# Kernel tuning notes

Hardware: AMD Instinct MI355X
Metric: run time of the kernel (lower is better)

The kernel has to match this reference:

```python
import jax, jax.numpy as jnp
import numpy as np

NB_NEIGHBORS = 8
RADIUS = 0.5
SPLIT = 32
FEATURE_SIZE = 128
OUTPUT_SIZE = 64
MIDDLE = (FEATURE_SIZE + OUTPUT_SIZE) // 2  # 96
N = 100000


def setup_inputs() -> dict:
    key = jax.random.key(0)
    ks = jax.random.split(key, 8)
    points = jax.random.normal(ks[0], (N, 3), dtype=jnp.float32)
    features = jax.random.normal(ks[1], (N, SPLIT + FEATURE_SIZE), dtype=jnp.float32)
    batch = jnp.sort(jax.random.randint(ks[2], (N,), 0, 16)).astype(jnp.int64)
    # neighborhood decoder modeled as Linear(split -> nb_neighbors*3)
    dec_W = jax.random.normal(ks[3], (SPLIT, NB_NEIGHBORS * 3), dtype=jnp.float32) / np.sqrt(SPLIT)
    dec_b = jnp.zeros((NB_NEIGHBORS * 3,), dtype=jnp.float32)
    fc1_W = jax.random.normal(ks[4], (FEATURE_SIZE + 3, MIDDLE), dtype=jnp.float32) / np.sqrt(FEATURE_SIZE + 3)
    fc1_b = jnp.zeros((MIDDLE,), dtype=jnp.float32)
    fc2_W = jax.random.normal(ks[5], (MIDDLE, OUTPUT_SIZE), dtype=jnp.float32) / np.sqrt(MIDDLE)
    fc2_b = jnp.zeros((OUTPUT_SIZE,), dtype=jnp.float32)
    return {"points": points, "features": features, "batch": batch,
            "dec_W": dec_W, "dec_b": dec_b,
            "fc1_W": fc1_W, "fc1_b": fc1_b,
            "fc2_W": fc2_W, "fc2_b": fc2_b}


def reference(points, features, batch, dec_W, dec_b, fc1_W, fc1_b, fc2_W, fc2_b):
    # split incoming features
    point_features = features[:, :SPLIT]            # [N, split] -> neighborhood decoder
    feature_features = features[:, SPLIT:]          # [N, feature_size]
    # neighborhood decoder: nb_neighbors relative 3-D points per input point
    relative_points = (point_features @ dec_W + dec_b).reshape(-1, 3)   # [N*nb, 3]
    output_batch = jnp.repeat(batch, NB_NEIGHBORS, axis=0)              # [N*nb]
    # gather features to each generated neighbor, concat with relative coords
    features_repeated = jnp.repeat(feature_features, NB_NEIGHBORS, axis=0)  # [N*nb, feature_size]
    concat_features = jnp.concatenate([relative_points, features_repeated], axis=1)  # [N*nb, 3+feature_size]
    # 2-layer MLP with ReLU
    fc1_features = jax.nn.relu(concat_features @ fc1_W + fc1_b)
    fc2_features = jax.nn.relu(fc1_features @ fc2_W + fc2_b)
    # scaled residual add onto anchor points
    anchor_points = jnp.repeat(points, NB_NEIGHBORS, axis=0)  # [N*nb, 3]
    output_points = anchor_points + relative_points * RADIUS
    return (output_points, fc2_features, output_batch)
```

## Files before the change

### kernel.cpp

```cpp
#include <hip/hip_runtime.h>

typedef __bf16 bf16x8 __attribute__((ext_vector_type(8)));
typedef float  f32x4  __attribute__((ext_vector_type(4)));

__device__ __forceinline__ ushort f2b(float f){
  union { float f; uint i; } v; v.f = f; uint u = v.i;
  return (ushort)((u + 0x7FFFu + ((u >> 16) & 1u)) >> 16);
}
__device__ __forceinline__ uint pack2(float a, float b){
  return (uint)f2b(a) | ((uint)f2b(b) << 16);
}
__device__ __forceinline__ bf16x8 ldfrag(const ushort* p){
  return *reinterpret_cast<const bf16x8*>(p);
}
__device__ __forceinline__ f32x4 relu4(f32x4 x){
  f32x4 r;
  r[0]=fmaxf(x[0],0.f); r[1]=fmaxf(x[1],0.f);
  r[2]=fmaxf(x[2],0.f); r[3]=fmaxf(x[3],0.f);
  return r;
}

__global__ void omd_transpose(const float* __restrict__ fc1W, const float* __restrict__ fc2W,
                              ushort* __restrict__ W1ftr, ushort* __restrict__ W2tr){
  int t = blockIdx.x * 256 + threadIdx.x;
  if (t < 96*128){
    int n = t >> 7, k = t & 127;
    W1ftr[t] = f2b(fc1W[(3 + k)*96 + n]);
  } else {
    int e = t - 96*128;
    if (e < 64*96){
      int n = e / 96, k = e - n*96;
      W2tr[e] = f2b(fc2W[k*64 + n]);
    }
  }
}

__global__ __launch_bounds__(256, 2) void omd_main(
    const float* __restrict__ points, const float* __restrict__ feats,
    const int*   __restrict__ batch,  const float* __restrict__ decW,
    const float* __restrict__ decb,   const float* __restrict__ fc1W,
    const float* __restrict__ fc1b,   const float* __restrict__ fc2b,
    const ushort* __restrict__ W1ftr, const ushort* __restrict__ W2tr,
    float* __restrict__ out, int npts)
{
  __shared__ __align__(16) float  pfL[32*32];
  __shared__ float decWL[32*24];
  __shared__ float decbL[24];
  __shared__ float w1pL[3*96];
  __shared__ float relL[32*24];
  __shared__ __align__(16) ushort ffL[32*136];
  __shared__ __align__(16) float  s1L[32*100];
  __shared__ __align__(16) ushort hL[2*32*104];

  const int t    = threadIdx.x;
  const int w    = t >> 6;
  const int lane = t & 63;
  const int q    = lane >> 4;
  const int c    = lane & 15;
  const int pbase = blockIdx.x * 32;

  const size_t offF = (size_t)npts * 24;
  const size_t offB = (size_t)npts * 24 + (size_t)npts * 512;

  {
    int p = t >> 3, v = t & 7;
    const f32x4* src = (const f32x4*)(feats + (size_t)(pbase + p)*160);
    ((f32x4*)pfL)[p*8 + v] = src[v];
  }
  {
    int m = t >> 3, seg = t & 7;
    const f32x4* src = (const f32x4*)(feats + (size_t)(pbase + m)*160 + 32 + seg*16);
    uint* dst = (uint*)(ffL + m*136 + seg*16);
    #pragma unroll
    for (int r = 0; r < 4; ++r){
      f32x4 f = src[r];
      dst[r*2    ] = pack2(f[0], f[1]);
      dst[r*2 + 1] = pack2(f[2], f[3]);
    }
  }
  for (int e = t; e < 768; e += 256) decWL[e] = decW[e];
  if (t < 24) decbL[t] = decb[t];
  for (int e = t; e < 288; e += 256) w1pL[e] = fc1W[e];

  bf16x8 w2f[4][3];
  #pragma unroll
  for (int nt = 0; nt < 4; ++nt)
    #pragma unroll
    for (int kt = 0; kt < 3; ++kt)
      w2f[nt][kt] = ldfrag(W2tr + (nt*16 + c)*96 + kt*32 + q*8);

  __syncthreads();

  #pragma unroll
  for (int oo = 0; oo < 3; ++oo){
    int o = t + 256*oo;
    int p = o / 24, col = o - p*24;
    float a = decbL[col];
    #pragma unroll
    for (int k = 0; k < 32; ++k)
      a += pfL[p*32 + k] * decWL[k*24 + col];
    relL[o] = a;
  }

  {
    int mt = w & 1, trio = w >> 1;
    const ushort* arow = ffL + (mt*16 + c)*136 + q*8;
    bf16x8 a0 = ldfrag(arow);
    bf16x8 a1 = ldfrag(arow + 32);
    bf16x8 a2 = ldfrag(arow + 64);
    bf16x8 a3 = ldfrag(arow + 96);
    #pragma unroll
    for (int i = 0; i < 3; ++i){
      const ushort* brow = W1ftr + ((trio*3 + i)*16 + c)*128 + q*8;
      f32x4 acc = {0.f, 0.f, 0.f, 0.f};
      acc = __builtin_amdgcn_mfma_f32_16x16x32_bf16(a0, ldfrag(brow      ), acc, 0, 0, 0);
      acc = __builtin_amdgcn_mfma_f32_16x16x32_bf16(a1, ldfrag(brow + 32 ), acc, 0, 0, 0);
      acc = __builtin_amdgcn_mfma_f32_16x16x32_bf16(a2, ldfrag(brow + 64 ), acc, 0, 0, 0);
      acc = __builtin_amdgcn_mfma_f32_16x16x32_bf16(a3, ldfrag(brow + 96 ), acc, 0, 0, 0);
      int col = (trio*3 + i)*16 + c;
      float bb = fc1b[col];
      #pragma unroll
      for (int r = 0; r < 4; ++r)
        s1L[(mt*16 + q*4 + r)*100 + col] = acc[r] + bb;
    }
  }
  __syncthreads();

  #pragma unroll 1
  for (int pair = 0; pair < 4; ++pair){
    {
      int m  = t >> 3;
      int jb = (t & 7) * 12;
      const f32x4* s1v = (const f32x4*)&s1L[m*100 + jb];
      f32x4 s0 = s1v[0], s1_ = s1v[1], s2 = s1v[2];
      f32x4 wa0 = *(const f32x4*)&w1pL[jb],     wa1 = *(const f32x4*)&w1pL[jb+4],     wa2 = *(const f32x4*)&w1pL[jb+8];
      f32x4 wb0 = *(const f32x4*)&w1pL[96+jb],  wb1 = *(const f32x4*)&w1pL[96+jb+4],  wb2 = *(const f32x4*)&w1pL[96+jb+8];
      f32x4 wc0 = *(const f32x4*)&w1pL[192+jb], wc1 = *(const f32x4*)&w1pL[192+jb+4], wc2 = *(const f32x4*)&w1pL[192+jb+8];
      uint* hLu = (uint*)hL;
      #pragma unroll
      for (int nl = 0; nl < 2; ++nl){
        int n = pair*2 + nl;
        float r0 = relL[m*24 + 3*n], r1 = relL[m*24 + 3*n + 1], r2 = relL[m*24 + 3*n + 2];
        f32x4 h0 = relu4(s0  + r0*wa0 + r1*wb0 + r2*wc0);
        f32x4 h1 = relu4(s1_ + r0*wa1 + r1*wb1 + r2*wc1);
        f32x4 h2 = relu4(s2  + r0*wa2 + r1*wb2 + r2*wc2);
        int ub = nl*1664 + m*52 + (t & 7)*6;
        hLu[ub    ] = pack2(h0[0], h0[1]);
        hLu[ub + 1] = pack2(h0[2], h0[3]);
        hLu[ub + 2] = pack2(h1[0], h1[1]);
        hLu[ub + 3] = pack2(h1[2], h1[3]);
        hLu[ub + 4] = pack2(h2[0], h2[1]);
        hLu[ub + 5] = pack2(h2[2], h2[3]);
      }
    }
    __syncthreads();

    {
      int nl = w & 1, mtw = w >> 1;
      const ushort* hrow = hL + nl*3328 + (mtw*16 + c)*104 + q*8;
      bf16x8 ha0 = ldfrag(hrow);
      bf16x8 ha1 = ldfrag(hrow + 32);
      bf16x8 ha2 = ldfrag(hrow + 64);
      int n = pair*2 + nl;
      int prow0 = pbase + mtw*16 + q*4;
      #pragma unroll
      for (int nt = 0; nt < 4; ++nt){
        float bb = fc2b[nt*16 + c];
        f32x4 acc = {bb, bb, bb, bb};
        acc = __builtin_amdgcn_mfma_f32_16x16x32_bf16(ha0, w2f[nt][0], acc, 0, 0, 0);
        acc = __builtin_amdgcn_mfma_f32_16x16x32_bf16(ha1, w2f[nt][1], acc, 0, 0, 0);
        acc = __builtin_amdgcn_mfma_f32_16x16x32_bf16(ha2, w2f[nt][2], acc, 0, 0, 0);
        #pragma unroll
        for (int r = 0; r < 4; ++r){
          size_t g = (size_t)(prow0 + r)*8 + n;
          out[offF + g*64 + nt*16 + c] = fmaxf(acc[r], 0.f);
        }
      }
    }
    __syncthreads();
  }

  #pragma unroll
  for (int i = 0; i < 3; ++i){
    int e = t + 256*i;
    int p = e / 24, rem = e - p*24;
    int d = rem % 3;
    float v = points[(size_t)(pbase + p)*3 + d] + 0.5f * relL[e];
    out[(size_t)(pbase + p)*24 + rem] = v;
  }
  {
    int p = t >> 3, n = t & 7;
    out[offB + (size_t)(pbase + p)*8 + n] = (float)batch[pbase + p];
  }
}

extern "C" void kernel_launch(void* const* d_in, const int* in_sizes, int n_in,
                              void* d_out, int out_size, void* d_ws, size_t ws_size,
                              hipStream_t stream){
  const float* points = (const float*)d_in[0];
  const float* feats  = (const float*)d_in[1];
  const int*   batch  = (const int*)d_in[2];
  const float* decW   = (const float*)d_in[3];
  const float* decb   = (const float*)d_in[4];
  const float* fc1W   = (const float*)d_in[5];
  const float* fc1b   = (const float*)d_in[6];
  const float* fc2W   = (const float*)d_in[7];
  const float* fc2b   = (const float*)d_in[8];
  float*  outp  = (float*)d_out;
  ushort* W1ftr = (ushort*)d_ws;
  ushort* W2tr  = W1ftr + 96*128;

  int npts = in_sizes[2];

  omd_transpose<<<72, 256, 0, stream>>>(fc1W, fc2W, W1ftr, W2tr);
  omd_main<<<npts/32, 256, 0, stream>>>(points, feats, batch, decW, decb,
                                        fc1W, fc1b, fc2b, W1ftr, W2tr,
                                        outp, npts);
}
```

Baseline: 309.4 us.

## Compute neighborhood decoder with bf16 MFMA and raise occupancy target

The 32x24 decoder projection is now done with one bf16 MFMA per wave instead of a scalar FP32 dot-product loop. To feed it, the decoder weights are transposed and padded to bf16 in the prep kernel and the point features are stored to LDS as bf16, which also reduces LDS usage. The per-pair s1/w1p loads are hoisted out of the loop, pack2 uses the HIP bf16x2 conversion intrinsic, and launch bounds ask for 3 blocks per CU. The relative points, which also feed the output coordinates, now carry bf16 rounding error, and the hoisted values add register pressure under the tighter launch bound.

```diff
diff --git a/kernel.cpp b/kernel.cpp
--- a/kernel.cpp
+++ b/kernel.cpp
@@ -1,4 +1,5 @@
 #include <hip/hip_runtime.h>
+#include <hip/hip_bf16.h>
 
 typedef __bf16 bf16x8 __attribute__((ext_vector_type(8)));
 typedef float  f32x4  __attribute__((ext_vector_type(4)));
@@ -8,7 +9,8 @@
   return (ushort)((u + 0x7FFFu + ((u >> 16) & 1u)) >> 16);
 }
 __device__ __forceinline__ uint pack2(float a, float b){
-  return (uint)f2b(a) | ((uint)f2b(b) << 16);
+  __hip_bfloat162 h = __float22bfloat162_rn(make_float2(a, b));
+  union { __hip_bfloat162 h; uint u; } v; v.h = h; return v.u;
 }
 __device__ __forceinline__ bf16x8 ldfrag(const ushort* p){
   return *reinterpret_cast<const bf16x8*>(p);
@@ -21,30 +23,33 @@
 }
 
 __global__ void omd_transpose(const float* __restrict__ fc1W, const float* __restrict__ fc2W,
-                              ushort* __restrict__ W1ftr, ushort* __restrict__ W2tr){
+                              const float* __restrict__ decW,
+                              ushort* __restrict__ W1ftr, ushort* __restrict__ W2tr,
+                              ushort* __restrict__ decWtr){
   int t = blockIdx.x * 256 + threadIdx.x;
   if (t < 96*128){
     int n = t >> 7, k = t & 127;
     W1ftr[t] = f2b(fc1W[(3 + k)*96 + n]);
-  } else {
+  } else if (t < 96*128 + 64*96){
     int e = t - 96*128;
-    if (e < 64*96){
-      int n = e / 96, k = e - n*96;
-      W2tr[e] = f2b(fc2W[k*64 + n]);
-    }
-  }
-}
-
-__global__ __launch_bounds__(256, 2) void omd_main(
+    int n = e / 96, k = e - n*96;
+    W2tr[e] = f2b(fc2W[k*64 + n]);
+  } else if (t < 96*128 + 64*96 + 32*32){
+    int e = t - (96*128 + 64*96);
+    int n = e >> 5, k = e & 31;
+    decWtr[e] = (n < 24) ? f2b(decW[k*24 + n]) : (ushort)0;
+  }
+}
+
+__global__ __launch_bounds__(256, 3) void omd_main(
     const float* __restrict__ points, const float* __restrict__ feats,
-    const int*   __restrict__ batch,  const float* __restrict__ decW,
-    const float* __restrict__ decb,   const float* __restrict__ fc1W,
-    const float* __restrict__ fc1b,   const float* __restrict__ fc2b,
-    const ushort* __restrict__ W1ftr, const ushort* __restrict__ W2tr,
+    const int*   __restrict__ batch,  const float* __restrict__ decb,
+    const float* __restrict__ fc1W,   const float* __restrict__ fc1b,
+    const float* __restrict__ fc2b,   const ushort* __restrict__ W1ftr,
+    const ushort* __restrict__ W2tr,  const ushort* __restrict__ decWtr,
     float* __restrict__ out, int npts)
 {
-  __shared__ __align__(16) float  pfL[32*32];
-  __shared__ float decWL[32*24];
+  __shared__ __align__(16) ushort pfB[32*40];
   __shared__ float decbL[24];
   __shared__ float w1pL[3*96];
   __shared__ float relL[32*24];
@@ -63,9 +68,12 @@
   const size_t offB = (size_t)npts * 24 + (size_t)npts * 512;
 
   {
-    int p = t >> 3, v = t & 7;
+    int p = t >> 3, seg = t & 7;
     const f32x4* src = (const f32x4*)(feats + (size_t)(pbase + p)*160);
-    ((f32x4*)pfL)[p*8 + v] = src[v];
+    f32x4 f = src[seg];
+    uint* dst = (uint*)pfB;
+    dst[p*20 + seg*2    ] = pack2(f[0], f[1]);
+    dst[p*20 + seg*2 + 1] = pack2(f[2], f[3]);
   }
   {
     int m = t >> 3, seg = t & 7;
@@ -78,7 +86,6 @@
       dst[r*2 + 1] = pack2(f[2], f[3]);
     }
   }
-  for (int e = t; e < 768; e += 256) decWL[e] = decW[e];
   if (t < 24) decbL[t] = decb[t];
   for (int e = t; e < 288; e += 256) w1pL[e] = fc1W[e];
 
@@ -91,15 +98,19 @@
 
   __syncthreads();
 
-  #pragma unroll
-  for (int oo = 0; oo < 3; ++oo){
-    int o = t + 256*oo;
-    int p = o / 24, col = o - p*24;
-    float a = decbL[col];
-    #pragma unroll
-    for (int k = 0; k < 32; ++k)
-      a += pfL[p*32 + k] * decWL[k*24 + col];
-    relL[o] = a;
+  {
+    int mt = w & 1, ntile = w >> 1;
+    bf16x8 a = ldfrag(pfB + (mt*16 + c)*40 + q*8);
+    bf16x8 b = ldfrag(decWtr + ((ntile*16 + c)<<5) + q*8);
+    f32x4 acc = {0.f, 0.f, 0.f, 0.f};
+    acc = __builtin_amdgcn_mfma_f32_16x16x32_bf16(a, b, acc, 0, 0, 0);
+    int n = ntile*16 + c;
+    if (n < 24){
+      float bb = decbL[n];
+      #pragma unroll
+      for (int r = 0; r < 4; ++r)
+        relL[(mt*16 + q*4 + r)*24 + n] = acc[r] + bb;
+    }
   }
 
   {
@@ -126,16 +137,20 @@
   }
   __syncthreads();
 
+  const int m  = t >> 3;
+  const int jb = (t & 7) * 12;
+  f32x4 s0, s1_, s2, wa0, wa1, wa2, wb0, wb1, wb2, wc0, wc1, wc2;
+  {
+    const f32x4* s1v = (const f32x4*)&s1L[m*100 + jb];
+    s0 = s1v[0]; s1_ = s1v[1]; s2 = s1v[2];
+    wa0 = *(const f32x4*)&w1pL[jb];     wa1 = *(const f32x4*)&w1pL[jb+4];     wa2 = *(const f32x4*)&w1pL[jb+8];
+    wb0 = *(const f32x4*)&w1pL[96+jb];  wb1 = *(const f32x4*)&w1pL[96+jb+4];  wb2 = *(const f32x4*)&w1pL[96+jb+8];
+    wc0 = *(const f32x4*)&w1pL[192+jb]; wc1 = *(const f32x4*)&w1pL[192+jb+4]; wc2 = *(const f32x4*)&w1pL[192+jb+8];
+  }
+
   #pragma unroll 1
   for (int pair = 0; pair < 4; ++pair){
     {
-      int m  = t >> 3;
-      int jb = (t & 7) * 12;
-      const f32x4* s1v = (const f32x4*)&s1L[m*100 + jb];
-      f32x4 s0 = s1v[0], s1_ = s1v[1], s2 = s1v[2];
-      f32x4 wa0 = *(const f32x4*)&w1pL[jb],     wa1 = *(const f32x4*)&w1pL[jb+4],     wa2 = *(const f32x4*)&w1pL[jb+8];
-      f32x4 wb0 = *(const f32x4*)&w1pL[96+jb],  wb1 = *(const f32x4*)&w1pL[96+jb+4],  wb2 = *(const f32x4*)&w1pL[96+jb+8];
-      f32x4 wc0 = *(const f32x4*)&w1pL[192+jb], wc1 = *(const f32x4*)&w1pL[192+jb+4], wc2 = *(const f32x4*)&w1pL[192+jb+8];
       uint* hLu = (uint*)hL;
       #pragma unroll
       for (int nl = 0; nl < 2; ++nl){
@@ -206,14 +221,15 @@
   const float* fc1b   = (const float*)d_in[6];
   const float* fc2W   = (const float*)d_in[7];
   const float* fc2b   = (const float*)d_in[8];
-  float*  outp  = (float*)d_out;
-  ushort* W1ftr = (ushort*)d_ws;
-  ushort* W2tr  = W1ftr + 96*128;
+  float*  outp   = (float*)d_out;
+  ushort* W1ftr  = (ushort*)d_ws;
+  ushort* W2tr   = W1ftr + 96*128;
+  ushort* decWtr = W2tr + 64*96;
 
   int npts = in_sizes[2];
 
-  omd_transpose<<<72, 256, 0, stream>>>(fc1W, fc2W, W1ftr, W2tr);
-  omd_main<<<npts/32, 256, 0, stream>>>(points, feats, batch, decW, decb,
-                                        fc1W, fc1b, fc2b, W1ftr, W2tr,
+  omd_transpose<<<76, 256, 0, stream>>>(fc1W, fc2W, decW, W1ftr, W2tr, decWtr);
+  omd_main<<<npts/32, 256, 0, stream>>>(points, feats, batch, decb,
+                                        fc1W, fc1b, fc2b, W1ftr, W2tr, decWtr,
                                         outp, npts);
 }
```

New measurement: 307.2 us. About the same (-0.7%).
